# Kernel optimization log

Measured on AMD Instinct MI355X. Metric: run time of the kernel, lower is better.

The kernel has to match this reference:

```python
import jax, jax.numpy as jnp
import numpy as np

N, E, C, Z, B, L = 50000, 800000, 32, 4, 8, 2
DEG = 16.0  # avg num neighbors = E / N


def ssp(x):
    # ShiftedSoftPlus
    return jax.nn.softplus(x) - jnp.log(2.0).astype(x.dtype)


def setup_inputs() -> dict:
    key = jax.random.key(0)
    ks = jax.random.split(key, 13)
    f32 = jnp.float32
    return {
        "node_features": jax.random.normal(ks[0], (N, 4 * C), f32),
        "node_attrs": jax.random.uniform(ks[1], (N, Z), f32),
        "edge_index": jax.random.randint(ks[2], (2, E), 0, N),
        "edge_embedding": jax.random.uniform(ks[3], (E, B), f32),
        "edge_attrs": jax.random.normal(ks[4], (E, 4), f32),
        "W0": jax.random.normal(ks[5], (L, C, C), f32) / np.sqrt(C),
        "W1": jax.random.normal(ks[6], (L, C, C), f32) / np.sqrt(C),
        "Wr1": jax.random.normal(ks[7], (L, B, B), f32) / np.sqrt(B),
        "Wr2": jax.random.normal(ks[8], (L, B, 5 * C), f32) / np.sqrt(B),
        "Ws": jax.random.normal(ks[9], (L, C, 2 * C), f32) / np.sqrt(C),
        "Wv": jax.random.normal(ks[10], (L, C, C), f32) / np.sqrt(C),
        "Wsc_s": jax.random.normal(ks[11], (L, C, Z, 2 * C), f32) / np.sqrt(C * Z),
        "Wsc_v": jax.random.normal(ks[12], (L, C, Z, C), f32) / np.sqrt(C * Z),
    }


def reference(node_features, node_attrs, edge_index, edge_embedding, edge_attrs,
              W0, W1, Wr1, Wr2, Ws, Wv, Wsc_s, Wsc_v):
    src, dst = edge_index[0], edge_index[1]
    Y0 = edge_attrs[:, :1]            # [E,1]  l=0 sph harmonic
    Yv = edge_attrs[:, 1:]            # [E,3]  l=1 sph harmonic
    x = node_features
    for l in range(L):
        s_in = x[:, :C]                          # [N,C]   scalars
        v_in = x[:, C:].reshape(N, C, 3)         # [N,C,3] vectors
        # linear (channel mixing per irrep)
        s = s_in @ W0[l]
        v = jnp.einsum('nci,cf->nfi', v_in, W1[l])
        # gather source node features per edge
        se = s[src]                              # [E,C]
        ve = v[src]                              # [E,C,3]
        # radial MLP -> per-edge tensor-product path weights (5 paths)
        w = jax.nn.silu(edge_embedding @ Wr1[l]) @ Wr2[l]   # [E,5C]
        w1, w2, w3, w4, w5 = jnp.split(w, 5, axis=-1)
        # tensor-product messages
        m_s = w1 * se * Y0 + w4 * jnp.einsum('eci,ei->ec', ve, Yv)          # 0ex0e->0e, 1ex1e->0e
        m_v = (w2[..., None] * se[..., None] * Yv[:, None, :]               # 0ex1e->1e
               + w3[..., None] * ve * Y0[..., None]                         # 1ex0e->1e
               + w5[..., None] * jnp.cross(ve, Yv[:, None, :]))             # 1ex1e->1e
        # scatter-sum to destination nodes, normalize by avg degree
        agg_s = jax.ops.segment_sum(m_s, dst, num_segments=N) / DEG
        agg_v = jax.ops.segment_sum(m_v, dst, num_segments=N) / DEG
        # output linear: scalars -> C feature scalars + C gates, vectors -> C
        out_s = agg_s @ Ws[l]                                               # [N,2C]
        out_v = jnp.einsum('nci,cf->nfi', agg_v, Wv[l])                     # [N,C,3]
        # self-connection (FullyConnectedTensorProduct with node_attrs)
        out_s = out_s + jnp.einsum('nc,nz,czf->nf', s_in, node_attrs, Wsc_s[l])
        out_v = out_v + jnp.einsum('nci,nz,czf->nfi', v_in, node_attrs, Wsc_v[l])
        # equivariant Gate nonlinearity
        feat = ssp(out_s[:, :C])
        gates = ssp(out_s[:, C:])
        gv = out_v * gates[..., None]
        new_x = jnp.concatenate([feat, gv.reshape(N, 3 * C)], axis=-1)
        x = x + new_x  # resnet (irreps match across layers)
    return x
```

## Files before the change

### kernel.cpp

```cpp
#include <hip/hip_runtime.h>
#include <math.h>

#define NN 50000
#define NE 800000
#define Cc 32
#define Zz 4
#define Bb 8
#define NL 2
#define DEG_INV (1.0f/16.0f)
#define SCAN_PAD 53248
#define EBLK (NE / 256)
#define NBLK (NN / 8)


__device__ __forceinline__ float ssp_f(float x) {
    float sp = fmaxf(x, 0.0f) + log1pf(expf(-fabsf(x)));
    return sp - 0.69314718055994530942f;
}
__device__ __forceinline__ float silu_f(float x) {
    return x / (1.0f + expf(-x));
}
__device__ __forceinline__ unsigned bf16rn(float f) {
    unsigned u = __float_as_uint(f);
    return (u + 0x7fffu + ((u >> 16) & 1u)) >> 16;
}


__global__ void hist_kernel(const int* __restrict__ ei, int* __restrict__ counts) {
    int e = blockIdx.x * 256 + threadIdx.x;
    if (e < NE) atomicAdd(&counts[ei[NE + e]], 1);
}

__global__ void scan_kernel(const int* __restrict__ counts,
                            int* __restrict__ base,
                            int* __restrict__ cursor) {
    __shared__ int partial[1024];
    int t = threadIdx.x;
    const int CH = 52;
    int b0 = t * CH;
    int sum = 0;
    #pragma unroll
    for (int i = 0; i < CH; i += 4) {
        int4 v = *(const int4*)(counts + b0 + i);
        sum += v.x + v.y + v.z + v.w;
    }
    partial[t] = sum;
    __syncthreads();
    for (int off = 1; off < 1024; off <<= 1) {
        int v = 0;
        if (t >= off) v = partial[t - off];
        __syncthreads();
        if (t >= off) partial[t] += v;
        __syncthreads();
    }
    int prefix = (t == 0) ? 0 : partial[t - 1];
    for (int i = b0; i < b0 + CH && i < NN; ++i) {
        base[i] = prefix;
        cursor[i] = prefix;
        prefix += counts[i];
    }
    if (t == 1023) base[NN] = partial[1023];
}

__global__ void prep_kernel(const int* __restrict__ ei,
                            const float* __restrict__ emb,
                            const float* __restrict__ eattr,
                            const float* __restrict__ Wr1,
                            int* __restrict__ cursor,
                            uint4* __restrict__ rec,
                            const float* __restrict__ nf,
                            const float* __restrict__ W0,
                            const float* __restrict__ W1,
                            float* __restrict__ x,
                            unsigned* __restrict__ svb) {
    __shared__ float wr1s[128];
    __shared__ float xs[8][128];
    int t = threadIdx.x;
    int b = blockIdx.x;
    if (b < EBLK) {
        if (t < 128) wr1s[t] = Wr1[t];
        __syncthreads();
        int e = b * 256 + t;
        int src = ei[e];
        int dst = ei[NE + e];
        int pos = atomicAdd(&cursor[dst], 1);

        const float4* s4 = (const float4*)emb + (size_t)e * 2;
        float4 a = s4[0], bb = s4[1];
        float em[8] = {a.x, a.y, a.z, a.w, bb.x, bb.y, bb.z, bb.w};
        float h0[8], h1[8];
        #pragma unroll
        for (int j = 0; j < 8; ++j) {
            float acc0 = 0.f, acc1 = 0.f;
            #pragma unroll
            for (int k = 0; k < 8; ++k) {
                acc0 = fmaf(em[k], wr1s[k * 8 + j], acc0);
                acc1 = fmaf(em[k], wr1s[64 + k * 8 + j], acc1);
            }
            h0[j] = silu_f(acc0);
            h1[j] = silu_f(acc1);
        }
        uint4 u0, u1;
        u0.x = bf16rn(h0[0]) | (bf16rn(h0[1]) << 16);
        u0.y = bf16rn(h0[2]) | (bf16rn(h0[3]) << 16);
        u0.z = bf16rn(h0[4]) | (bf16rn(h0[5]) << 16);
        u0.w = bf16rn(h0[6]) | (bf16rn(h0[7]) << 16);
        u1.x = bf16rn(h1[0]) | (bf16rn(h1[1]) << 16);
        u1.y = bf16rn(h1[2]) | (bf16rn(h1[3]) << 16);
        u1.z = bf16rn(h1[4]) | (bf16rn(h1[5]) << 16);
        u1.w = bf16rn(h1[6]) | (bf16rn(h1[7]) << 16);
        uint4* r = rec + (size_t)pos * 4;
        r[0] = u0;
        r[1] = u1;
        r[2] = ((const uint4*)eattr)[e];
        r[3] = make_uint4((unsigned)src, 0u, 0u, 0u);
    } else {
        int node0 = (b - EBLK) * 8;
        #pragma unroll
        for (int k = 0; k < 4; ++k) {
            int idx = t + k * 256;
            int n = idx >> 7, col = idx & 127;
            float val = nf[(size_t)(node0 + n) * 128 + col];
            xs[n][col] = val;
            x[(size_t)(node0 + n) * 128 + col] = val;
        }
        __syncthreads();
        int n = t >> 5, f = t & 31;
        int gn = node0 + n;
        float acc_s = 0.f, a0 = 0.f, a1 = 0.f, a2 = 0.f;
        #pragma unroll
        for (int c = 0; c < Cc; ++c) {
            float w0 = W0[c * Cc + f];
            float w1 = W1[c * Cc + f];
            acc_s = fmaf(xs[n][c], w0, acc_s);
            a0 = fmaf(xs[n][32 + c * 3 + 0], w1, a0);
            a1 = fmaf(xs[n][32 + c * 3 + 1], w1, a1);
            a2 = fmaf(xs[n][32 + c * 3 + 2], w1, a2);
        }
        unsigned* o = svb + (size_t)gn * 64;
        o[f]      = bf16rn(acc_s) | (bf16rn(a0) << 16);
        o[32 + f] = bf16rn(a1)    | (bf16rn(a2) << 16);
    }
}

#define PROC_EDGE_PK(ua, Yv, se, v0, v1, v2)                                 \
    do {                                                                     \
        float hh0 = __uint_as_float(ua.x << 16);                             \
        float hh1 = __uint_as_float(ua.x & 0xffff0000u);                     \
        float hh2 = __uint_as_float(ua.y << 16);                             \
        float hh3 = __uint_as_float(ua.y & 0xffff0000u);                     \
        float hh4 = __uint_as_float(ua.z << 16);                             \
        float hh5 = __uint_as_float(ua.z & 0xffff0000u);                     \
        float hh6 = __uint_as_float(ua.w << 16);                             \
        float hh7 = __uint_as_float(ua.w & 0xffff0000u);                     \
        float w1 = 0.f, w2 = 0.f, w3 = 0.f, w4 = 0.f, w5 = 0.f;              \
        w1 = fmaf(hh0, wr2s[0][c], w1); w2 = fmaf(hh0, wr2s[0][32 + c], w2); \
        w3 = fmaf(hh0, wr2s[0][64 + c], w3); w4 = fmaf(hh0, wr2s[0][96 + c], w4); \
        w5 = fmaf(hh0, wr2s[0][128 + c], w5);                                \
        w1 = fmaf(hh1, wr2s[1][c], w1); w2 = fmaf(hh1, wr2s[1][32 + c], w2); \
        w3 = fmaf(hh1, wr2s[1][64 + c], w3); w4 = fmaf(hh1, wr2s[1][96 + c], w4); \
        w5 = fmaf(hh1, wr2s[1][128 + c], w5);                                \
        w1 = fmaf(hh2, wr2s[2][c], w1); w2 = fmaf(hh2, wr2s[2][32 + c], w2); \
        w3 = fmaf(hh2, wr2s[2][64 + c], w3); w4 = fmaf(hh2, wr2s[2][96 + c], w4); \
        w5 = fmaf(hh2, wr2s[2][128 + c], w5);                                \
        w1 = fmaf(hh3, wr2s[3][c], w1); w2 = fmaf(hh3, wr2s[3][32 + c], w2); \
        w3 = fmaf(hh3, wr2s[3][64 + c], w3); w4 = fmaf(hh3, wr2s[3][96 + c], w4); \
        w5 = fmaf(hh3, wr2s[3][128 + c], w5);                                \
        w1 = fmaf(hh4, wr2s[4][c], w1); w2 = fmaf(hh4, wr2s[4][32 + c], w2); \
        w3 = fmaf(hh4, wr2s[4][64 + c], w3); w4 = fmaf(hh4, wr2s[4][96 + c], w4); \
        w5 = fmaf(hh4, wr2s[4][128 + c], w5);                                \
        w1 = fmaf(hh5, wr2s[5][c], w1); w2 = fmaf(hh5, wr2s[5][32 + c], w2); \
        w3 = fmaf(hh5, wr2s[5][64 + c], w3); w4 = fmaf(hh5, wr2s[5][96 + c], w4); \
        w5 = fmaf(hh5, wr2s[5][128 + c], w5);                                \
        w1 = fmaf(hh6, wr2s[6][c], w1); w2 = fmaf(hh6, wr2s[6][32 + c], w2); \
        w3 = fmaf(hh6, wr2s[6][64 + c], w3); w4 = fmaf(hh6, wr2s[6][96 + c], w4); \
        w5 = fmaf(hh6, wr2s[6][128 + c], w5);                                \
        w1 = fmaf(hh7, wr2s[7][c], w1); w2 = fmaf(hh7, wr2s[7][32 + c], w2); \
        w3 = fmaf(hh7, wr2s[7][64 + c], w3); w4 = fmaf(hh7, wr2s[7][96 + c], w4); \
        w5 = fmaf(hh7, wr2s[7][128 + c], w5);                                \
        float dot = v0 * Yv.y + v1 * Yv.z + v2 * Yv.w;                       \
        ms += w1 * se * Yv.x + w4 * dot;                                     \
        float cx = v1 * Yv.w - v2 * Yv.z;                                    \
        float cy = v2 * Yv.y - v0 * Yv.w;                                    \
        float cz = v0 * Yv.z - v1 * Yv.y;                                    \
        mv0 += w2 * se * Yv.y + w3 * v0 * Yv.x + w5 * cx;                    \
        mv1 += w2 * se * Yv.z + w3 * v1 * Yv.x + w5 * cy;                    \
        mv2 += w2 * se * Yv.w + w3 * v2 * Yv.x + w5 * cz;                    \
    } while (0)

#define UNPACK_SV(p, se, v0, v1, v2)                                         \
    unsigned ulo_##se = (p)[c], uhi_##se = (p)[32 + c];                      \
    float se = __uint_as_float(ulo_##se << 16);                              \
    float v0 = __uint_as_float(ulo_##se & 0xffff0000u);                      \
    float v1 = __uint_as_float(uhi_##se << 16);                              \
    float v2 = __uint_as_float(uhi_##se & 0xffff0000u)

__global__ void agg_kernel(const int* __restrict__ base,
                           const uint4* __restrict__ rec,
                           const int lsel,
                           const unsigned* __restrict__ svb,
                           const float* __restrict__ Wr2,
                           float* __restrict__ agg) {
    __shared__ float wr2s[8][160];
    int t = threadIdx.x;
    for (int i = t; i < 8 * 160; i += 256) ((float*)wr2s)[i] = Wr2[i];
    __syncthreads();
    int n = blockIdx.x * 8 + (t >> 5);
    int c = t & 31;
    int jb = base[n], je = base[n + 1];
    float ms = 0.f, mv0 = 0.f, mv1 = 0.f, mv2 = 0.f;

    int j = jb;
    for (; j + 1 < je; j += 2) {
        const uint4* rA = rec + (size_t)j * 4;
        const uint4* rB = rA + 4;
        uint4 uA = rA[lsel];
        float4 YA = *(const float4*)(rA + 2);
        int srcA = (int)rA[3].x;
        uint4 uB = rB[lsel];
        float4 YB = *(const float4*)(rB + 2);
        int srcB = (int)rB[3].x;
        const unsigned* pA = svb + (size_t)srcA * 64;
        const unsigned* pB = svb + (size_t)srcB * 64;
        UNPACK_SV(pA, seA, vA0, vA1, vA2);
        UNPACK_SV(pB, seB, vB0, vB1, vB2);
        PROC_EDGE_PK(uA, YA, seA, vA0, vA1, vA2);
        PROC_EDGE_PK(uB, YB, seB, vB0, vB1, vB2);
    }
    if (j < je) {
        const uint4* rA = rec + (size_t)j * 4;
        uint4 uA = rA[lsel];
        float4 YA = *(const float4*)(rA + 2);
        int srcA = (int)rA[3].x;
        const unsigned* pA = svb + (size_t)srcA * 64;
        UNPACK_SV(pA, seA, vA0, vA1, vA2);
        PROC_EDGE_PK(uA, YA, seA, vA0, vA1, vA2);
    }

    float* ap = agg + (size_t)n * 128;
    ap[c]      = ms * DEG_INV;
    ap[32 + c] = mv0 * DEG_INV;
    ap[64 + c] = mv1 * DEG_INV;
    ap[96 + c] = mv2 * DEG_INV;
}

template <int WANT_SV>
__global__ void post_pre_kernel(float* __restrict__ x,
                                const float* __restrict__ attrs,
                                const float* __restrict__ agg,
                                const float* __restrict__ Ws,
                                const float* __restrict__ Wv,
                                const float* __restrict__ Wsc_s,
                                const float* __restrict__ Wsc_v,
                                const float* __restrict__ W0n,
                                const float* __restrict__ W1n,
                                unsigned* __restrict__ svb) {
    __shared__ float shx[16][128];
    __shared__ float sha[16][128];
    int t = threadIdx.x;
    int node0 = blockIdx.x * 16;
    #pragma unroll
    for (int k = 0; k < 4; ++k) {
        int f4 = t + k * 128;
        int n = f4 >> 5, col4 = f4 & 31;
        int gn = node0 + n;
        if (gn < NN) {
            ((float4*)&shx[n][0])[col4] = ((const float4*)(x + (size_t)gn * 128))[col4];
            ((float4*)&sha[n][0])[col4] = ((const float4*)(agg + (size_t)gn * 128))[col4];
        }
    }
    __syncthreads();
    int g = t >> 5, f = t & 31;

    float az[4][4];
    #pragma unroll
    for (int k = 0; k < 4; ++k) {
        int gn = node0 + g + k * 4;
        if (gn < NN) {
            float4 a4 = ((const float4*)attrs)[gn];
            az[k][0] = a4.x; az[k][1] = a4.y; az[k][2] = a4.z; az[k][3] = a4.w;
        } else {
            az[k][0] = az[k][1] = az[k][2] = az[k][3] = 0.f;
        }
    }

    float os0[4] = {0, 0, 0, 0}, os1[4] = {0, 0, 0, 0};
    float ov0[4] = {0, 0, 0, 0}, ov1[4] = {0, 0, 0, 0}, ov2[4] = {0, 0, 0, 0};

    #pragma unroll 2
    for (int c = 0; c < Cc; ++c) {
        float ws0 = Ws[c * 64 + f];
        float ws1 = Ws[c * 64 + 32 + f];
        float wv  = Wv[c * 32 + f];
        #pragma unroll
        for (int k = 0; k < 4; ++k) {
            int n = g + k * 4;
            float as  = sha[n][c];
            float av0 = sha[n][32 + c];
            float av1 = sha[n][64 + c];
            float av2 = sha[n][96 + c];
            os0[k] = fmaf(as, ws0, os0[k]);
            os1[k] = fmaf(as, ws1, os1[k]);
            ov0[k] = fmaf(av0, wv, ov0[k]);
            ov1[k] = fmaf(av1, wv, ov1[k]);
            ov2[k] = fmaf(av2, wv, ov2[k]);
        }
        #pragma unroll
        for (int z = 0; z < 4; ++z) {
            int cz = c * 4 + z;
            float wss0 = Wsc_s[cz * 64 + f];
            float wss1 = Wsc_s[cz * 64 + 32 + f];
            float wsv  = Wsc_v[cz * 32 + f];
            #pragma unroll
            for (int k = 0; k < 4; ++k) {
                int n = g + k * 4;
                float azv = az[k][z];
                float sa = shx[n][c] * azv;
                os0[k] = fmaf(sa, wss0, os0[k]);
                os1[k] = fmaf(sa, wss1, os1[k]);
                float va = azv * wsv;
                ov0[k] = fmaf(shx[n][32 + c * 3 + 0], va, ov0[k]);
                ov1[k] = fmaf(shx[n][32 + c * 3 + 1], va, ov1[k]);
                ov2[k] = fmaf(shx[n][32 + c * 3 + 2], va, ov2[k]);
            }
        }
    }

    float ns[4], nv0[4], nv1[4], nv2[4];
    #pragma unroll
    for (int k = 0; k < 4; ++k) {
        int n = g + k * 4;
        int gn = node0 + n;
        float feat = ssp_f(os0[k]);
        float gate = ssp_f(os1[k]);
        ns[k]  = shx[n][f] + feat;
        nv0[k] = shx[n][32 + f * 3 + 0] + ov0[k] * gate;
        nv1[k] = shx[n][32 + f * 3 + 1] + ov1[k] * gate;
        nv2[k] = shx[n][32 + f * 3 + 2] + ov2[k] * gate;
        if (gn < NN) {
            float* xp = x + (size_t)gn * 128;
            xp[f] = ns[k];
            xp[32 + f * 3 + 0] = nv0[k];
            xp[32 + f * 3 + 1] = nv1[k];
            xp[32 + f * 3 + 2] = nv2[k];
        }
    }

    if (WANT_SV) {
        __syncthreads();
        #pragma unroll
        for (int k = 0; k < 4; ++k) {
            int n = g + k * 4;
            sha[n][f] = ns[k];
            sha[n][32 + f * 3 + 0] = nv0[k];
            sha[n][32 + f * 3 + 1] = nv1[k];
            sha[n][32 + f * 3 + 2] = nv2[k];
        }
        __syncthreads();
        float bs[4] = {0, 0, 0, 0};
        float b0[4] = {0, 0, 0, 0}, b1[4] = {0, 0, 0, 0}, b2[4] = {0, 0, 0, 0};
        #pragma unroll 4
        for (int c = 0; c < Cc; ++c) {
            float w0 = W0n[c * Cc + f];
            float w1 = W1n[c * Cc + f];
            #pragma unroll
            for (int k = 0; k < 4; ++k) {
                int n = g + k * 4;
                bs[k] = fmaf(sha[n][c], w0, bs[k]);
                b0[k] = fmaf(sha[n][32 + c * 3 + 0], w1, b0[k]);
                b1[k] = fmaf(sha[n][32 + c * 3 + 1], w1, b1[k]);
                b2[k] = fmaf(sha[n][32 + c * 3 + 2], w1, b2[k]);
            }
        }
        #pragma unroll
        for (int k = 0; k < 4; ++k) {
            int gn = node0 + g + k * 4;
            if (gn < NN) {
                unsigned* o = svb + (size_t)gn * 64;
                o[f]      = bf16rn(bs[k]) | (bf16rn(b0[k]) << 16);
                o[32 + f] = bf16rn(b1[k]) | (bf16rn(b2[k]) << 16);
            }
        }
    }
}

__global__ void edge_atomic_kernel(const int* __restrict__ ei,
                                   const float* __restrict__ emb,
                                   const float* __restrict__ eattr,
                                   const unsigned* __restrict__ svb,
                                   const float* __restrict__ Wr1,
                                   const float* __restrict__ Wr2,
                                   float* __restrict__ agg) {
    int t = threadIdx.x;
    int eg = t >> 5;
    int c = t & 31;
    int e = blockIdx.x * 8 + eg;
    if (e >= NE) return;
    int src = ei[e];
    int dst = ei[NE + e];
    float h = 0.f;
    if (c < 8) {
        #pragma unroll
        for (int k = 0; k < 8; ++k)
            h = fmaf(emb[e * 8 + k], Wr1[k * 8 + c], h);
        h = silu_f(h);
    }
    float w1 = 0.f, w2 = 0.f, w3 = 0.f, w4 = 0.f, w5 = 0.f;
    #pragma unroll
    for (int j = 0; j < 8; ++j) {
        float hj = __shfl(h, j, 32);
        const float* wr = Wr2 + j * 160;
        w1 = fmaf(hj, wr[c], w1);
        w2 = fmaf(hj, wr[32 + c], w2);
        w3 = fmaf(hj, wr[64 + c], w3);
        w4 = fmaf(hj, wr[96 + c], w4);
        w5 = fmaf(hj, wr[128 + c], w5);
    }
    float Y0  = eattr[e * 4 + 0];
    float Yv0 = eattr[e * 4 + 1];
    float Yv1 = eattr[e * 4 + 2];
    float Yv2 = eattr[e * 4 + 3];
    const unsigned* p = svb + (size_t)src * 64;
    unsigned ulo = p[c], uhi = p[32 + c];
    float se  = __uint_as_float(ulo << 16);
    float ve0 = __uint_as_float(ulo & 0xffff0000u);
    float ve1 = __uint_as_float(uhi << 16);
    float ve2 = __uint_as_float(uhi & 0xffff0000u);
    float dot = ve0 * Yv0 + ve1 * Yv1 + ve2 * Yv2;
    float msg = (w1 * se * Y0 + w4 * dot) * DEG_INV;
    float cx = ve1 * Yv2 - ve2 * Yv1;
    float cy = ve2 * Yv0 - ve0 * Yv2;
    float cz = ve0 * Yv1 - ve1 * Yv0;
    float mv0 = (w2 * se * Yv0 + w3 * ve0 * Y0 + w5 * cx) * DEG_INV;
    float mv1 = (w2 * se * Yv1 + w3 * ve1 * Y0 + w5 * cy) * DEG_INV;
    float mv2 = (w2 * se * Yv2 + w3 * ve2 * Y0 + w5 * cz) * DEG_INV;
    float* ap = agg + (size_t)dst * 128;
    atomicAdd(&ap[c], msg);
    atomicAdd(&ap[32 + c], mv0);
    atomicAdd(&ap[64 + c], mv1);
    atomicAdd(&ap[96 + c], mv2);
}

__global__ void init_kernel(const float* __restrict__ nf,
                            const float* __restrict__ W0,
                            const float* __restrict__ W1,
                            float* __restrict__ x,
                            unsigned* __restrict__ svb) {
    __shared__ float xs[8][128];
    int t = threadIdx.x;
    int node0 = blockIdx.x * 8;
    #pragma unroll
    for (int k = 0; k < 4; ++k) {
        int idx = t + k * 256;
        int n = idx >> 7, col = idx & 127;
        float val = nf[(size_t)(node0 + n) * 128 + col];
        xs[n][col] = val;
        x[(size_t)(node0 + n) * 128 + col] = val;
    }
    __syncthreads();
    int n = t >> 5, f = t & 31;
    int gn = node0 + n;
    float acc_s = 0.f, a0 = 0.f, a1 = 0.f, a2 = 0.f;
    #pragma unroll
    for (int c = 0; c < Cc; ++c) {
        float w0 = W0[c * Cc + f];
        float w1 = W1[c * Cc + f];
        acc_s = fmaf(xs[n][c], w0, acc_s);
        a0 = fmaf(xs[n][32 + c * 3 + 0], w1, a0);
        a1 = fmaf(xs[n][32 + c * 3 + 1], w1, a1);
        a2 = fmaf(xs[n][32 + c * 3 + 2], w1, a2);
    }
    unsigned* o = svb + (size_t)gn * 64;
    o[f]      = bf16rn(acc_s) | (bf16rn(a0) << 16);
    o[32 + f] = bf16rn(a1)    | (bf16rn(a2) << 16);
}

extern "C" void kernel_launch(void* const* d_in, const int* in_sizes, int n_in,
                              void* d_out, int out_size, void* d_ws, size_t ws_size,
                              hipStream_t stream) {
    const float* node_features  = (const float*)d_in[0];
    const float* node_attrs     = (const float*)d_in[1];
    const int*   edge_index     = (const int*)d_in[2];
    const float* edge_embedding = (const float*)d_in[3];
    const float* edge_attrs     = (const float*)d_in[4];
    const float* W0    = (const float*)d_in[5];
    const float* W1    = (const float*)d_in[6];
    const float* Wr1   = (const float*)d_in[7];
    const float* Wr2   = (const float*)d_in[8];
    const float* Ws    = (const float*)d_in[9];
    const float* Wv    = (const float*)d_in[10];
    const float* Wsc_s = (const float*)d_in[11];
    const float* Wsc_v = (const float*)d_in[12];

    float* x = (float*)d_out;

    float* ws = (float*)d_ws;
    unsigned* svb = (unsigned*)ws;
    float* agg  = (float*)(svb + (size_t)NN * 64);
    uint4* rec  = (uint4*)(agg + (size_t)NN * 128);
    int* counts   = (int*)(rec + (size_t)NE * 4);
    int* base     = counts + SCAN_PAD;
    int* cursor   = base + NN + 1;
    size_t needed = ((char*)(cursor + NN)) - (char*)d_ws;

    bool use_sorted = ws_size >= needed;
    const int PP_GRID = (NN + 15) / 16;

    if (use_sorted) {
        hipMemsetAsync(counts, 0, SCAN_PAD * sizeof(int), stream);
        hist_kernel<<<NE / 256, 256, 0, stream>>>(edge_index, counts);
        scan_kernel<<<1, 1024, 0, stream>>>(counts, base, cursor);
        prep_kernel<<<EBLK + NBLK, 256, 0, stream>>>(
            edge_index, edge_embedding, edge_attrs, Wr1,
            cursor, rec,
            node_features, W0, W1, x, svb);

        agg_kernel<<<NN / 8, 256, 0, stream>>>(base, rec, 0, svb, Wr2, agg);
        post_pre_kernel<1><<<PP_GRID, 128, 0, stream>>>(
            x, node_attrs, agg, Ws, Wv, Wsc_s, Wsc_v,
            W0 + Cc * Cc, W1 + Cc * Cc, svb);
        agg_kernel<<<NN / 8, 256, 0, stream>>>(base, rec, 1, svb,
                                               Wr2 + Bb * 5 * Cc, agg);
        post_pre_kernel<0><<<PP_GRID, 128, 0, stream>>>(
            x, node_attrs, agg,
            Ws + Cc * 2 * Cc, Wv + Cc * Cc,
            Wsc_s + Cc * Zz * 2 * Cc, Wsc_v + Cc * Zz * Cc,
            nullptr, nullptr, nullptr);
    } else {
        hipMemcpyAsync(x, node_features, (size_t)NN * 128 * sizeof(float),
                       hipMemcpyDeviceToDevice, stream);
        for (int l = 0; l < NL; ++l) {
            hipMemsetAsync(agg, 0, (size_t)NN * 128 * sizeof(float), stream);
            init_kernel<<<NN / 8, 256, 0, stream>>>(
                x, W0 + l * Cc * Cc, W1 + l * Cc * Cc, x, svb);
            edge_atomic_kernel<<<NE / 8, 256, 0, stream>>>(
                edge_index, edge_embedding, edge_attrs, svb,
                Wr1 + l * Bb * Bb, Wr2 + l * Bb * 5 * Cc, agg);
            post_pre_kernel<0><<<PP_GRID, 128, 0, stream>>>(
                x, node_attrs, agg,
                Ws + l * Cc * 2 * Cc, Wv + l * Cc * Cc,
                Wsc_s + l * Cc * Zz * 2 * Cc, Wsc_v + l * Cc * Zz * Cc,
                nullptr, nullptr, nullptr);
        }
    }
}
```

Baseline: 533.1 us.

## Replace single-block prefix scan with three-pass multi-block scan

The single 1024-thread scan block, which did serial 52-element per-thread loops and a shared-memory Hillis-Steele scan, is replaced by three kernels. The first takes per-block partial sums, the second runs a wavefront shuffle scan of the block sums, and the third does the final per-block shuffle scan and writes base and cursor. This spreads the scan across 49 blocks with coalesced int4 accesses instead of strided serial writes from one CU. It adds two kernel launches and hardcodes base[NN]=NE.

Result: faster. 440.4 us (-17.4%).

```diff
diff --git a/kernel.cpp b/kernel.cpp
--- a/kernel.cpp
+++ b/kernel.cpp
@@ -9,6 +9,7 @@
 #define NL 2
 #define DEG_INV (1.0f/16.0f)
 #define SCAN_PAD 53248
+#define SCAN_BLOCKS 49
 #define EBLK (NE / 256)
 #define NBLK (NN / 8)
 
@@ -31,35 +32,62 @@
     if (e < NE) atomicAdd(&counts[ei[NE + e]], 1);
 }
 
-__global__ void scan_kernel(const int* __restrict__ counts,
-                            int* __restrict__ base,
-                            int* __restrict__ cursor) {
-    __shared__ int partial[1024];
-    int t = threadIdx.x;
-    const int CH = 52;
-    int b0 = t * CH;
-    int sum = 0;
-    #pragma unroll
-    for (int i = 0; i < CH; i += 4) {
-        int4 v = *(const int4*)(counts + b0 + i);
-        sum += v.x + v.y + v.z + v.w;
-    }
-    partial[t] = sum;
+__global__ void scan_part_kernel(const int* __restrict__ counts,
+                                 int* __restrict__ blocksum) {
+    __shared__ int red[256];
+    int b = blockIdx.x, t = threadIdx.x;
+    int4 v = ((const int4*)counts)[b * 256 + t];
+    red[t] = v.x + v.y + v.z + v.w;
     __syncthreads();
-    for (int off = 1; off < 1024; off <<= 1) {
-        int v = 0;
-        if (t >= off) v = partial[t - off];
+    for (int off = 128; off > 0; off >>= 1) {
+        if (t < off) red[t] += red[t + off];
         __syncthreads();
-        if (t >= off) partial[t] += v;
-        __syncthreads();
-    }
-    int prefix = (t == 0) ? 0 : partial[t - 1];
-    for (int i = b0; i < b0 + CH && i < NN; ++i) {
-        base[i] = prefix;
-        cursor[i] = prefix;
-        prefix += counts[i];
-    }
-    if (t == 1023) base[NN] = partial[1023];
+    }
+    if (t == 0) blocksum[b] = red[0];
+}
+
+__global__ void scan_top_kernel(int* __restrict__ blocksum,
+                                int* __restrict__ base) {
+    int lane = threadIdx.x;
+    int v = (lane < SCAN_BLOCKS) ? blocksum[lane] : 0;
+    int inc = v;
+    #pragma unroll
+    for (int off = 1; off < 64; off <<= 1) {
+        int n = __shfl_up(inc, off, 64);
+        if (lane >= off) inc += n;
+    }
+    if (lane < SCAN_BLOCKS) blocksum[lane] = inc - v;
+    if (lane == 0) base[NN] = NE;
+}
+
+__global__ void scan_fin_kernel(const int* __restrict__ counts,
+                                const int* __restrict__ blockoff,
+                                int* __restrict__ base,
+                                int* __restrict__ cursor) {
+    __shared__ int wsum[4];
+    int b = blockIdx.x, t = threadIdx.x;
+    int4 v = ((const int4*)counts)[b * 256 + t];
+    int s = v.x + v.y + v.z + v.w;
+    int lane = t & 63, wid = t >> 6;
+    int inc = s;
+    #pragma unroll
+    for (int off = 1; off < 64; off <<= 1) {
+        int n = __shfl_up(inc, off, 64);
+        if (lane >= off) inc += n;
+    }
+    if (lane == 63) wsum[wid] = inc;
+    __syncthreads();
+    int add = blockoff[b];
+    for (int w = 0; w < wid; ++w) add += wsum[w];
+    int e0 = inc - s + add;
+    int e1 = e0 + v.x;
+    int e2 = e1 + v.y;
+    int e3 = e2 + v.z;
+    int idx = b * 1024 + t * 4;
+    if (idx + 0 < NN) { base[idx + 0] = e0; cursor[idx + 0] = e0; }
+    if (idx + 1 < NN) { base[idx + 1] = e1; cursor[idx + 1] = e1; }
+    if (idx + 2 < NN) { base[idx + 2] = e2; cursor[idx + 2] = e2; }
+    if (idx + 3 < NN) { base[idx + 3] = e3; cursor[idx + 3] = e3; }
 }
 
 __global__ void prep_kernel(const int* __restrict__ ei,
@@ -501,7 +529,8 @@
     int* counts   = (int*)(rec + (size_t)NE * 4);
     int* base     = counts + SCAN_PAD;
     int* cursor   = base + NN + 1;
-    size_t needed = ((char*)(cursor + NN)) - (char*)d_ws;
+    int* blocksum = cursor + NN;
+    size_t needed = ((char*)(blocksum + SCAN_BLOCKS)) - (char*)d_ws;
 
     bool use_sorted = ws_size >= needed;
     const int PP_GRID = (NN + 15) / 16;
@@ -509,7 +538,10 @@
     if (use_sorted) {
         hipMemsetAsync(counts, 0, SCAN_PAD * sizeof(int), stream);
         hist_kernel<<<NE / 256, 256, 0, stream>>>(edge_index, counts);
-        scan_kernel<<<1, 1024, 0, stream>>>(counts, base, cursor);
+        scan_part_kernel<<<SCAN_BLOCKS, 256, 0, stream>>>(counts, blocksum);
+        scan_top_kernel<<<1, 64, 0, stream>>>(blocksum, base);
+        scan_fin_kernel<<<SCAN_BLOCKS, 256, 0, stream>>>(counts, blocksum,
+                                                         base, cursor);
         prep_kernel<<<EBLK + NBLK, 256, 0, stream>>>(
             edge_index, edge_embedding, edge_attrs, Wr1,
             cursor, rec,
```
